# Optimization experiments

Measured on AMD Instinct MI355X. Metric: run time of the kernel, lower is better.

The kernel has to match this reference:

```python
import jax, jax.numpy as jnp
import numpy as np
import math

B, C, H, W = 16, 256, 48, 48
CK = C // 8


def setup_inputs() -> dict:
    key = jax.random.key(0)
    ks = jax.random.split(key, 8)
    s = 0.05
    return {
        "x": jax.random.normal(ks[0], (B, C, H, W), dtype=jnp.float32),
        "Wq": jax.random.normal(ks[1], (CK, C), dtype=jnp.float32) * s,
        "bq": jax.random.normal(ks[2], (CK,), dtype=jnp.float32) * s,
        "Wk": jax.random.normal(ks[3], (CK, C), dtype=jnp.float32) * s,
        "bk": jax.random.normal(ks[4], (CK,), dtype=jnp.float32) * s,
        "Wv": jax.random.normal(ks[5], (C, C), dtype=jnp.float32) * s,
        "bv": jax.random.normal(ks[6], (C,), dtype=jnp.float32) * s,
        "gamma": jax.random.normal(ks[7], (1,), dtype=jnp.float32) * 0.1,
    }


def reference(x, Wq, bq, Wk, bk, Wv, bv, gamma):
    b, c, h, w = x.shape
    n = h * w
    xf = x.reshape(b, c, n)  # [B, C, N] (1x1 conv == channel matmul)
    q = jnp.einsum("oc,bcn->bno", Wq, xf) + bq  # [B, N, C/8]
    k = jnp.einsum("oc,bcn->bon", Wk, xf) + bk[None, :, None]  # [B, C/8, N]
    v = jnp.einsum("oc,bcn->bon", Wv, xf) + bv[None, :, None]  # [B, C, N]
    # NOTE: original scales by sqrt(C) (d_k = C), not sqrt(C//8)
    energy = jnp.einsum("bnd,bdm->bnm", q, k) / math.sqrt(c)  # [B, N, N]
    attn = jax.nn.softmax(energy, axis=-1)
    # out[b,c,i] = sum_j v[b,c,j] * attn[b,i,j]
    out = jnp.einsum("bcj,bij->bci", v, attn).reshape(b, c, h, w)
    return gamma[0] * out + x
```

## Files before the change

kernel.cpp:

```cpp
#include <hip/hip_runtime.h>
#include <hip/hip_bf16.h>

#define Bn  16
#define Cn  256
#define CKn 32
#define Nn  2304

typedef __attribute__((ext_vector_type(16))) float f32x16;
typedef __attribute__((ext_vector_type(8)))  short bf16x8;
typedef __attribute__((ext_vector_type(4)))  int   i32x4;

union FragU { unsigned u[4]; bf16x8 v; };
union KU    { i32x4 i; bf16x8 v; };

__device__ __forceinline__ unsigned pk(float lo, float hi){
  unsigned a = (unsigned)__bfloat16_as_ushort(__float2bfloat16(lo));
  unsigned b = (unsigned)__bfloat16_as_ushort(__float2bfloat16(hi));
  return a | (b << 16);
}

__device__ __forceinline__ void halfswap(unsigned A, unsigned Bv, int ,
                                         unsigned &w0, unsigned &w2){
  asm("v_permlane32_swap_b32 %0, %1" : "+v"(A), "+v"(Bv));
  w0 = A; w2 = Bv;
}

__device__ __forceinline__ void conv_store(const f32x16& a, int h, int l,
                                           __hip_bfloat16* dst0, size_t stride){
  unsigned Wp[8];
  #pragma unroll
  for (int q = 0; q < 8; ++q) Wp[q] = pk(a[2*q], a[2*q+1]);
  #pragma unroll
  for (int k2 = 0; k2 < 2; ++k2){
    FragU u;
    halfswap(Wp[4*k2+0], Wp[4*k2+2], h, u.u[0], u.u[2]);
    halfswap(Wp[4*k2+1], Wp[4*k2+3], h, u.u[1], u.u[3]);
    *(bf16x8*)(dst0 + k2*stride + l*8) = u.v;
  }
}

__device__ __forceinline__ void gld16(const void* g, void* l){
  __builtin_amdgcn_global_load_lds(
      (__attribute__((address_space(1))) void*)const_cast<void*>(g),
      (__attribute__((address_space(3))) void*)l, 16, 0, 0);
}

__global__ __launch_bounds__(64) void wfrag_kernel(
    const float* __restrict__ Wq, const float* __restrict__ bq,
    const float* __restrict__ Wk, const float* __restrict__ bk,
    const float* __restrict__ Wv, const float* __restrict__ bv,
    __hip_bfloat16* __restrict__ Wf){
  const int kt = blockIdx.x / 10, tile = blockIdx.x % 10;
  const int l = threadIdx.x, lo = l & 31, h = l >> 5;
  __hip_bfloat16* dst = Wf + (size_t)(kt*10 + tile)*512 + l*8;
  if (kt < 16){
    const float* Wp; int row;
    if (tile < 8)       { Wp = Wv; row = tile*32 + lo; }
    else if (tile == 8) { Wp = Wq; row = lo; }
    else                { Wp = Wk; row = lo; }
    #pragma unroll
    for (int e = 0; e < 8; ++e)
      dst[e] = __float2bfloat16(Wp[(size_t)row*Cn + kt*16 + 8*h + e]);
  } else {
    const float* bp = tile < 8 ? bv : (tile == 8 ? bq : bk);
    int row = tile < 8 ? tile*32 + lo : lo;
    #pragma unroll
    for (int e = 0; e < 8; ++e)
      dst[e] = __float2bfloat16((h == 0 && e == 0) ? bp[row] : 0.f);
  }
}

__global__ __launch_bounds__(256) void proj_kernel(
    const float* __restrict__ x, const __hip_bfloat16* __restrict__ Wf,
    __hip_bfloat16* __restrict__ Qf, __hip_bfloat16* __restrict__ Kf,
    __hip_bfloat16* __restrict__ Vf){
  const int u = blockIdx.x*4 + (threadIdx.x >> 6);
  const int b = u / 72, n32 = u % 72;
  const int l = threadIdx.x & 63, lo = l & 31, h = l >> 5;
  const int n0 = n32*32;

  f32x16 acc[10];
  #pragma unroll
  for (int t = 0; t < 10; ++t)
    #pragma unroll
    for (int r = 0; r < 16; ++r) acc[t][r] = 0.f;

  const float* xb = x + (size_t)b*Cn*Nn + n0 + lo;

  #pragma unroll 1
  for (int kt = 0; kt < 16; ++kt){
    FragU xf;
    float v[8];
    #pragma unroll
    for (int e = 0; e < 8; ++e) v[e] = xb[(size_t)(kt*16 + 8*h + e)*Nn];
    #pragma unroll
    for (int q = 0; q < 4; ++q) xf.u[q] = pk(v[2*q], v[2*q+1]);
    const __hip_bfloat16* wfp = Wf + (size_t)(kt*10)*512 + l*8;
    #pragma unroll
    for (int t = 0; t < 10; ++t){
      bf16x8 wf = *(const bf16x8*)(wfp + t*512);
      if (t < 8) acc[t] = __builtin_amdgcn_mfma_f32_32x32x16_bf16(xf.v, wf, acc[t], 0,0,0);
      else       acc[t] = __builtin_amdgcn_mfma_f32_32x32x16_bf16(wf, xf.v, acc[t], 0,0,0);
    }
  }
  {
    FragU xf;
    xf.u[0] = h ? 0u : 0x00003f80u;
    xf.u[1] = xf.u[2] = xf.u[3] = 0u;
    const __hip_bfloat16* wfp = Wf + (size_t)(16*10)*512 + l*8;
    #pragma unroll
    for (int t = 0; t < 10; ++t){
      bf16x8 wf = *(const bf16x8*)(wfp + t*512);
      if (t < 8) acc[t] = __builtin_amdgcn_mfma_f32_32x32x16_bf16(xf.v, wf, acc[t], 0,0,0);
      else       acc[t] = __builtin_amdgcn_mfma_f32_32x32x16_bf16(wf, xf.v, acc[t], 0,0,0);
    }
  }

  #pragma unroll
  for (int r = 0; r < 16; ++r) acc[8][r] *= 0.09016844f;

  #pragma unroll
  for (int t = 0; t < 8; ++t)
    conv_store(acc[t], h, l, Vf + (((size_t)b*144 + n32*2)*8 + t)*512, 8*512);
  conv_store(acc[8], h, l, Qf + ((size_t)b*72 + n32)*2*512, 512);
  conv_store(acc[9], h, l, Kf + ((size_t)b*72 + n32)*2*512, 512);
}

__global__ __launch_bounds__(256, 3) void attn_kernel(
    const __hip_bfloat16* __restrict__ Qf, const __hip_bfloat16* __restrict__ Kf,
    const __hip_bfloat16* __restrict__ Vf, const float* __restrict__ x,
    const float* __restrict__ gptr, float* __restrict__ out){
  __shared__ __align__(16) char smem[49152];
  const int xcd = blockIdx.x & 7, seq = blockIdx.x >> 3;
  const int b    = xcd*2 + (seq / 36);
  const int rem  = seq % 36;
  const int q128 = rem >> 1;
  const int ch   = rem & 1;
  const int tid = threadIdx.x;
  const int w = tid >> 6, l = tid & 63, lo = l & 31, h = l >> 5;

  auto stageV = [&](int jt, int buf){
    #pragma unroll
    for (int r = 0; r < 4; ++r){
      const char* gV = (const char*)Vf
          + ((size_t)((b*144 + jt*4 + r)*8 + ch*4 + (tid >> 6)))*1024
          + (size_t)(tid & 63)*16;
      gld16(gV, smem + buf*16384 + r*4096 + w*1024);
    }
  };
  auto kload = [&](int jn, KU (&kf)[2][2]){
    const char* ka = (const char*)Kf + (size_t)(b*72 + jn*2)*2048 + (size_t)l*16;
    asm volatile("global_load_dwordx4 %0, %1, off"             : "=v"(kf[0][0].i) : "v"(ka) : "memory");
    asm volatile("global_load_dwordx4 %0, %1, off offset:1024" : "=v"(kf[0][1].i) : "v"(ka) : "memory");
    asm volatile("global_load_dwordx4 %0, %1, off offset:2048" : "=v"(kf[1][0].i) : "v"(ka) : "memory");
    asm volatile("global_load_dwordx4 %0, %1, off offset:3072" : "=v"(kf[1][1].i) : "v"(ka) : "memory");
  };

  bf16x8 qf[2];
  #pragma unroll
  for (int kt = 0; kt < 2; ++kt)
    qf[kt] = *(const bf16x8*)(Qf + (((size_t)b*72 + q128*4 + w)*2 + kt)*512 + l*8);

  KU kfA[2][2], kfB[2][2];
  kload(0, kfA);
  stageV(0, 0);
  stageV(1, 1);

  f32x16 acc[2];
  #pragma unroll
  for (int c = 0; c < 2; ++c)
    #pragma unroll
    for (int r = 0; r < 16; ++r) acc[c][r] = 0.f;
  float lsum = 0.f;

  auto body = [&](int jt, int vb, KU (&cur)[2][2], KU (&nxt)[2][2]){
    asm volatile("s_waitcnt vmcnt(4)" ::: "memory");
    __builtin_amdgcn_s_barrier();
    __builtin_amdgcn_sched_barrier(0);

    int jn = jt + 1; if (jn >= 36) jn -= 36;
    kload(jn, nxt);
    int j2 = jt + 2; if (j2 >= 36) j2 -= 36;
    int sb = vb + 2;  if (sb >= 3)  sb -= 3;
    stageV(j2, sb);

    f32x16 z;
    #pragma unroll
    for (int r = 0; r < 16; ++r) z[r] = 0.f;
    f32x16 S0 = __builtin_amdgcn_mfma_f32_32x32x16_bf16(cur[0][0].v, qf[0], z, 0,0,0);
    S0 = __builtin_amdgcn_mfma_f32_32x32x16_bf16(cur[0][1].v, qf[1], S0, 0,0,0);
    f32x16 S1 = __builtin_amdgcn_mfma_f32_32x32x16_bf16(cur[1][0].v, qf[0], z, 0,0,0);
    S1 = __builtin_amdgcn_mfma_f32_32x32x16_bf16(cur[1][1].v, qf[1], S1, 0,0,0);

    FragU pf[4];
    float sadd = 0.f;
    {
      unsigned Wp[8];
      #pragma unroll
      for (int q = 0; q < 8; ++q){
        float p0 = exp2f(S0[2*q]);
        float p1 = exp2f(S0[2*q+1]);
        sadd += p0 + p1; Wp[q] = pk(p0, p1);
      }
      halfswap(Wp[0], Wp[2], h, pf[0].u[0], pf[0].u[2]);
      halfswap(Wp[1], Wp[3], h, pf[0].u[1], pf[0].u[3]);
      halfswap(Wp[4], Wp[6], h, pf[1].u[0], pf[1].u[2]);
      halfswap(Wp[5], Wp[7], h, pf[1].u[1], pf[1].u[3]);
    }
    {
      unsigned Wp[8];
      #pragma unroll
      for (int q = 0; q < 8; ++q){
        float p0 = exp2f(S1[2*q]);
        float p1 = exp2f(S1[2*q+1]);
        sadd += p0 + p1; Wp[q] = pk(p0, p1);
      }
      halfswap(Wp[0], Wp[2], h, pf[2].u[0], pf[2].u[2]);
      halfswap(Wp[1], Wp[3], h, pf[2].u[1], pf[2].u[3]);
      halfswap(Wp[4], Wp[6], h, pf[3].u[0], pf[3].u[2]);
      halfswap(Wp[5], Wp[7], h, pf[3].u[1], pf[3].u[3]);
    }
    lsum += sadd;

    const char* cbV = smem + vb*16384;
    #pragma unroll
    for (int js = 0; js < 4; ++js){
      #pragma unroll
      for (int c = 0; c < 2; ++c){
        bf16x8 v = *(const bf16x8*)(cbV + (js*4 + (2*0 + c) + 0)*1024 + l*16);
        (void)v;
      }
    }
  };
  (void)body;

  f32x16 acc4[4];
  #pragma unroll
  for (int c = 0; c < 4; ++c)
    #pragma unroll
    for (int r = 0; r < 16; ++r) acc4[c][r] = 0.f;

  auto body2 = [&](int jt, int vb, KU (&cur)[2][2], KU (&nxt)[2][2]){
    asm volatile("s_waitcnt vmcnt(4)" ::: "memory");
    __builtin_amdgcn_s_barrier();
    __builtin_amdgcn_sched_barrier(0);

    int jn = jt + 1; if (jn >= 36) jn -= 36;
    kload(jn, nxt);
    int j2 = jt + 2; if (j2 >= 36) j2 -= 36;
    int sb = vb + 2;  if (sb >= 3)  sb -= 3;
    stageV(j2, sb);

    f32x16 z;
    #pragma unroll
    for (int r = 0; r < 16; ++r) z[r] = 0.f;
    f32x16 S0 = __builtin_amdgcn_mfma_f32_32x32x16_bf16(cur[0][0].v, qf[0], z, 0,0,0);
    S0 = __builtin_amdgcn_mfma_f32_32x32x16_bf16(cur[0][1].v, qf[1], S0, 0,0,0);
    f32x16 S1 = __builtin_amdgcn_mfma_f32_32x32x16_bf16(cur[1][0].v, qf[0], z, 0,0,0);
    S1 = __builtin_amdgcn_mfma_f32_32x32x16_bf16(cur[1][1].v, qf[1], S1, 0,0,0);

    FragU pf[4];
    float sadd = 0.f;
    {
      unsigned Wp[8];
      #pragma unroll
      for (int q = 0; q < 8; ++q){
        float p0 = exp2f(S0[2*q]);
        float p1 = exp2f(S0[2*q+1]);
        sadd += p0 + p1; Wp[q] = pk(p0, p1);
      }
      halfswap(Wp[0], Wp[2], h, pf[0].u[0], pf[0].u[2]);
      halfswap(Wp[1], Wp[3], h, pf[0].u[1], pf[0].u[3]);
      halfswap(Wp[4], Wp[6], h, pf[1].u[0], pf[1].u[2]);
      halfswap(Wp[5], Wp[7], h, pf[1].u[1], pf[1].u[3]);
    }
    {
      unsigned Wp[8];
      #pragma unroll
      for (int q = 0; q < 8; ++q){
        float p0 = exp2f(S1[2*q]);
        float p1 = exp2f(S1[2*q+1]);
        sadd += p0 + p1; Wp[q] = pk(p0, p1);
      }
      halfswap(Wp[0], Wp[2], h, pf[2].u[0], pf[2].u[2]);
      halfswap(Wp[1], Wp[3], h, pf[2].u[1], pf[2].u[3]);
      halfswap(Wp[4], Wp[6], h, pf[3].u[0], pf[3].u[2]);
      halfswap(Wp[5], Wp[7], h, pf[3].u[1], pf[3].u[3]);
    }
    lsum += sadd;

    const char* cbV = smem + vb*16384;
    #pragma unroll
    for (int js = 0; js < 4; ++js){
      #pragma unroll
      for (int c = 0; c < 4; ++c){
        bf16x8 v = *(const bf16x8*)(cbV + (js*4 + c)*1024 + l*16);
        acc4[c] = __builtin_amdgcn_mfma_f32_32x32x16_bf16(v, pf[js].v, acc4[c], 0,0,0);
      }
    }
  };

  int vb = 0;
  #pragma unroll 1
  for (int jt = 0; jt < 36; jt += 2){
    body2(jt, vb, kfA, kfB);
    int vb1 = vb + 1; if (vb1 == 3) vb1 = 0;
    body2(jt + 1, vb1, kfB, kfA);
    vb = vb1 + 1; if (vb == 3) vb = 0;
  }

  lsum += __shfl_xor(lsum, 32);
  const float sc = gptr[0] / lsum;
  const int ibase = q128*128 + w*32;
  #pragma unroll
  for (int c = 0; c < 4; ++c){
    #pragma unroll
    for (int r = 0; r < 16; ++r){
      const int cg = ch*128 + c*32 + (r & 3) + 8*(r >> 2) + 4*h;
      const size_t idx = ((size_t)b*Cn + cg)*Nn + ibase + lo;
      out[idx] = acc4[c][r]*sc + x[idx];
    }
  }
}

extern "C" void kernel_launch(void* const* d_in, const int* in_sizes, int n_in,
                              void* d_out, int out_size, void* d_ws, size_t ws_size,
                              hipStream_t stream) {
  const float* x     = (const float*)d_in[0];
  const float* Wq    = (const float*)d_in[1];
  const float* bq    = (const float*)d_in[2];
  const float* Wk    = (const float*)d_in[3];
  const float* bk    = (const float*)d_in[4];
  const float* Wv    = (const float*)d_in[5];
  const float* bv    = (const float*)d_in[6];
  const float* gamma = (const float*)d_in[7];
  float* out = (float*)d_out;

  __hip_bfloat16* Qf = (__hip_bfloat16*)d_ws;
  __hip_bfloat16* Kf = Qf + (size_t)Bn*72*2*512;
  __hip_bfloat16* Vf = Kf + (size_t)Bn*72*2*512;
  __hip_bfloat16* Wf = Vf + (size_t)Bn*144*8*512;

  wfrag_kernel<<<dim3(170), dim3(64), 0, stream>>>(Wq, bq, Wk, bk, Wv, bv, Wf);
  proj_kernel<<<dim3(288), dim3(256), 0, stream>>>(x, Wf, Qf, Kf, Vf);
  attn_kernel<<<dim3(576), dim3(256), 0, stream>>>(Qf, Kf, Vf, x, gamma, out);
}
```

Baseline: 125.9 us.

## Software-pipeline QK^T of the next tile with PV of the current tile

Restructures the attention main loop so each iteration computes the QK scores for tile j+1 while issuing the PV MFMAs for tile j, whose probabilities were computed in the previous iteration. K fragments are now prefetched two tiles ahead, with a prologue that computes the first softmax and an epilogue that drains the last PV. The goal is to hide the exp/pack/permlane softmax latency behind the matrix-core work. In exchange it keeps a second set of probability fragments live, which raises register pressure, and the vmcnt wait counts have to be exactly right.

```diff
diff --git a/kernel.cpp b/kernel.cpp
--- a/kernel.cpp
+++ b/kernel.cpp
@@ -161,38 +161,14 @@
   for (int kt = 0; kt < 2; ++kt)
     qf[kt] = *(const bf16x8*)(Qf + (((size_t)b*72 + q128*4 + w)*2 + kt)*512 + l*8);
 
-  KU kfA[2][2], kfB[2][2];
-  kload(0, kfA);
-  stageV(0, 0);
-  stageV(1, 1);
-
-  f32x16 acc[2];
-  #pragma unroll
-  for (int c = 0; c < 2; ++c)
-    #pragma unroll
-    for (int r = 0; r < 16; ++r) acc[c][r] = 0.f;
+  f32x16 acc4[4];
+  #pragma unroll
+  for (int c = 0; c < 4; ++c)
+    #pragma unroll
+    for (int r = 0; r < 16; ++r) acc4[c][r] = 0.f;
   float lsum = 0.f;
 
-  auto body = [&](int jt, int vb, KU (&cur)[2][2], KU (&nxt)[2][2]){
-    asm volatile("s_waitcnt vmcnt(4)" ::: "memory");
-    __builtin_amdgcn_s_barrier();
-    __builtin_amdgcn_sched_barrier(0);
-
-    int jn = jt + 1; if (jn >= 36) jn -= 36;
-    kload(jn, nxt);
-    int j2 = jt + 2; if (j2 >= 36) j2 -= 36;
-    int sb = vb + 2;  if (sb >= 3)  sb -= 3;
-    stageV(j2, sb);
-
-    f32x16 z;
-    #pragma unroll
-    for (int r = 0; r < 16; ++r) z[r] = 0.f;
-    f32x16 S0 = __builtin_amdgcn_mfma_f32_32x32x16_bf16(cur[0][0].v, qf[0], z, 0,0,0);
-    S0 = __builtin_amdgcn_mfma_f32_32x32x16_bf16(cur[0][1].v, qf[1], S0, 0,0,0);
-    f32x16 S1 = __builtin_amdgcn_mfma_f32_32x32x16_bf16(cur[1][0].v, qf[0], z, 0,0,0);
-    S1 = __builtin_amdgcn_mfma_f32_32x32x16_bf16(cur[1][1].v, qf[1], S1, 0,0,0);
-
-    FragU pf[4];
+  auto softmax = [&](const f32x16& S0, const f32x16& S1, FragU (&pf)[4]){
     float sadd = 0.f;
     {
       unsigned Wp[8];
@@ -221,74 +197,17 @@
       halfswap(Wp[5], Wp[7], h, pf[3].u[1], pf[3].u[3]);
     }
     lsum += sadd;
-
-    const char* cbV = smem + vb*16384;
-    #pragma unroll
-    for (int js = 0; js < 4; ++js){
-      #pragma unroll
-      for (int c = 0; c < 2; ++c){
-        bf16x8 v = *(const bf16x8*)(cbV + (js*4 + (2*0 + c) + 0)*1024 + l*16);
-        (void)v;
-      }
-    }
-  };
-  (void)body;
-
-  f32x16 acc4[4];
-  #pragma unroll
-  for (int c = 0; c < 4; ++c)
-    #pragma unroll
-    for (int r = 0; r < 16; ++r) acc4[c][r] = 0.f;
-
-  auto body2 = [&](int jt, int vb, KU (&cur)[2][2], KU (&nxt)[2][2]){
-    asm volatile("s_waitcnt vmcnt(4)" ::: "memory");
-    __builtin_amdgcn_s_barrier();
-    __builtin_amdgcn_sched_barrier(0);
-
-    int jn = jt + 1; if (jn >= 36) jn -= 36;
-    kload(jn, nxt);
-    int j2 = jt + 2; if (j2 >= 36) j2 -= 36;
-    int sb = vb + 2;  if (sb >= 3)  sb -= 3;
-    stageV(j2, sb);
-
+  };
+  auto qk = [&](KU (&kf)[2][2], f32x16& S0, f32x16& S1){
     f32x16 z;
     #pragma unroll
     for (int r = 0; r < 16; ++r) z[r] = 0.f;
-    f32x16 S0 = __builtin_amdgcn_mfma_f32_32x32x16_bf16(cur[0][0].v, qf[0], z, 0,0,0);
-    S0 = __builtin_amdgcn_mfma_f32_32x32x16_bf16(cur[0][1].v, qf[1], S0, 0,0,0);
-    f32x16 S1 = __builtin_amdgcn_mfma_f32_32x32x16_bf16(cur[1][0].v, qf[0], z, 0,0,0);
-    S1 = __builtin_amdgcn_mfma_f32_32x32x16_bf16(cur[1][1].v, qf[1], S1, 0,0,0);
-
-    FragU pf[4];
-    float sadd = 0.f;
-    {
-      unsigned Wp[8];
-      #pragma unroll
-      for (int q = 0; q < 8; ++q){
-        float p0 = exp2f(S0[2*q]);
-        float p1 = exp2f(S0[2*q+1]);
-        sadd += p0 + p1; Wp[q] = pk(p0, p1);
-      }
-      halfswap(Wp[0], Wp[2], h, pf[0].u[0], pf[0].u[2]);
-      halfswap(Wp[1], Wp[3], h, pf[0].u[1], pf[0].u[3]);
-      halfswap(Wp[4], Wp[6], h, pf[1].u[0], pf[1].u[2]);
-      halfswap(Wp[5], Wp[7], h, pf[1].u[1], pf[1].u[3]);
-    }
-    {
-      unsigned Wp[8];
-      #pragma unroll
-      for (int q = 0; q < 8; ++q){
-        float p0 = exp2f(S1[2*q]);
-        float p1 = exp2f(S1[2*q+1]);
-        sadd += p0 + p1; Wp[q] = pk(p0, p1);
-      }
-      halfswap(Wp[0], Wp[2], h, pf[2].u[0], pf[2].u[2]);
-      halfswap(Wp[1], Wp[3], h, pf[2].u[1], pf[2].u[3]);
-      halfswap(Wp[4], Wp[6], h, pf[3].u[0], pf[3].u[2]);
-      halfswap(Wp[5], Wp[7], h, pf[3].u[1], pf[3].u[3]);
-    }
-    lsum += sadd;
-
+    S0 = __builtin_amdgcn_mfma_f32_32x32x16_bf16(kf[0][0].v, qf[0], z, 0,0,0);
+    S0 = __builtin_amdgcn_mfma_f32_32x32x16_bf16(kf[0][1].v, qf[1], S0, 0,0,0);
+    S1 = __builtin_amdgcn_mfma_f32_32x32x16_bf16(kf[1][0].v, qf[0], z, 0,0,0);
+    S1 = __builtin_amdgcn_mfma_f32_32x32x16_bf16(kf[1][1].v, qf[1], S1, 0,0,0);
+  };
+  auto pv = [&](FragU (&pf)[4], int vb){
     const char* cbV = smem + vb*16384;
     #pragma unroll
     for (int js = 0; js < 4; ++js){
@@ -300,14 +219,48 @@
     }
   };
 
+  KU kfA[2][2], kfB[2][2];
+  FragU pfA[4], pfB[4];
+
+  kload(0, kfA);
+  kload(1, kfB);
+  stageV(0, 0);
+  stageV(1, 1);
+  asm volatile("s_waitcnt vmcnt(12)" ::: "memory");
+  __builtin_amdgcn_sched_barrier(0);
+  {
+    f32x16 S0, S1;
+    qk(kfA, S0, S1);
+    softmax(S0, S1, pfA);
+  }
+
+  auto body = [&](int jt, KU (&kq)[2][2], KU (&kl)[2][2],
+                  FragU (&pfu)[4], FragU (&pfw)[4], int vb){
+    asm volatile("s_waitcnt vmcnt(4)" ::: "memory");
+    __builtin_amdgcn_s_barrier();
+    __builtin_amdgcn_sched_barrier(0);
+    int j2 = jt + 2; if (j2 >= 36) j2 -= 36;
+    kload(j2, kl);
+    int sb = vb + 2; if (sb >= 3) sb -= 3;
+    stageV(j2, sb);
+    f32x16 S0, S1;
+    qk(kq, S0, S1);
+    pv(pfu, vb);
+    softmax(S0, S1, pfw);
+  };
+
   int vb = 0;
   #pragma unroll 1
-  for (int jt = 0; jt < 36; jt += 2){
-    body2(jt, vb, kfA, kfB);
-    int vb1 = vb + 1; if (vb1 == 3) vb1 = 0;
-    body2(jt + 1, vb1, kfB, kfA);
-    vb = vb1 + 1; if (vb == 3) vb = 0;
-  }
+  for (int jt = 0; jt < 34; jt += 2){
+    body(jt,   kfB, kfA, pfA, pfB, vb); vb = (vb == 2) ? 0 : vb + 1;
+    body(jt+1, kfA, kfB, pfB, pfA, vb); vb = (vb == 2) ? 0 : vb + 1;
+  }
+  body(34, kfB, kfA, pfA, pfB, vb); vb = (vb == 2) ? 0 : vb + 1;
+
+  asm volatile("s_waitcnt vmcnt(8)" ::: "memory");
+  __builtin_amdgcn_s_barrier();
+  __builtin_amdgcn_sched_barrier(0);
+  pv(pfB, vb);
 
   lsum += __shfl_xor(lsum, 32);
   const float sc = gptr[0] / lsum;
```

Measured after the change: 132.9 us. +5.6%, slower.
